# Kernel tuning notes

Measured on AMD Instinct MI355X. Metric: run time of the kernel, lower is better.

Reference implementation:

```python
import jax, jax.numpy as jnp
import numpy as np

B, T, D = 2, 512, 512
UNITS, H = 512, 8
DEPTH = UNITS // H  # 64


def setup_inputs() -> dict:
    key = jax.random.key(0)
    ks = jax.random.split(key, 16)
    s = 0.05  # keras 'random_normal' initializer stddev
    inp = {
        "query": jax.random.normal(ks[0], (B, T, D), jnp.float32),
        "key": jax.random.normal(ks[1], (B, T, D), jnp.float32),
        "value": jax.random.normal(ks[2], (B, T, D), jnp.float32),
        # input projections (Dense(units) with bias)
        "Wq": jax.random.normal(ks[3], (D, UNITS), jnp.float32) * s,
        "bq": jnp.zeros((UNITS,), jnp.float32),
        "Wk": jax.random.normal(ks[4], (D, UNITS), jnp.float32) * s,
        "bk": jnp.zeros((UNITS,), jnp.float32),
        "Wv": jax.random.normal(ks[5], (D, UNITS), jnp.float32) * s,
        "bv": jnp.zeros((UNITS,), jnp.float32),
        # per-head additive-attention params, stacked over heads
        "Wq_h": jax.random.normal(ks[6], (H, DEPTH, DEPTH), jnp.float32) * s,
        "Wk_h": jax.random.normal(ks[7], (H, DEPTH, DEPTH), jnp.float32) * s,
        "va_h": jax.random.normal(ks[8], (H, DEPTH), jnp.float32) * s,
        "b_h": jnp.zeros((H, DEPTH), jnp.float32),
        # output projection
        "Wo": jax.random.normal(ks[9], (UNITS, UNITS), jnp.float32) * s,
        "bo": jnp.zeros((UNITS,), jnp.float32),
    }
    return inp


def _split_heads(x):
    b = x.shape[0]
    return x.reshape(b, -1, H, DEPTH).transpose(0, 2, 1, 3)  # [B,H,T,depth]


def reference(query, key, value, Wq, bq, Wk, bk, Wv, bv,
              Wq_h, Wk_h, va_h, b_h, Wo, bo):
    Q = _split_heads(query @ Wq + bq)  # [B,H,T,d]
    K = _split_heads(key @ Wk + bk)    # [B,H,S,d]
    V = _split_heads(value @ Wv + bv)  # computed but unused, as in original

    # per-head linear maps for additive scores
    q = jnp.einsum("bhtd,hde->bhte", Q, Wq_h)
    k = jnp.einsum("bhsd,hde->bhse", K, Wk_h)
    # Bahdanau additive score: tanh(q_t + k_s + b) . v_a, summed over depth
    feat = jnp.tanh(q[:, :, :, None, :] + k[:, :, None, :, :]
                    + b_h[None, :, None, None, :])  # [B,H,T,S,d]
    score = jnp.einsum("bhtse,he->bhts", feat, va_h)  # [B,H,T,S]
    attn = jax.nn.softmax(score, axis=-1)
    # original multiplies by KEY (not value)
    heads = jnp.einsum("bhts,bhsd->bhtd", attn, K)  # [B,H,T,d]
    merged = heads.transpose(0, 2, 1, 3).reshape(query.shape[0], -1, UNITS)
    return merged @ Wo + bo
```

## Files before the change

### kernel.cpp

```cpp
#include <hip/hip_runtime.h>
#include <hip/hip_bf16.h>

#define T_SEQ 512
#define NH 8
#define DEPTH 64
#define UNITS_ 512
#define SCALE2 2.8853900817779268f
#define LOG2E 1.4426950408889634f

typedef __attribute__((ext_vector_type(8))) short short8;
typedef __attribute__((ext_vector_type(4))) float floatx4;

__global__ __launch_bounds__(256) void qk_head_fused(
    const float* __restrict__ query, const float* __restrict__ key,
    const float* __restrict__ Wq, const float* __restrict__ bq,
    const float* __restrict__ Wk, const float* __restrict__ bk,
    const float* __restrict__ Wq_h, const float* __restrict__ Wk_h,
    const float* __restrict__ bh,
    float* __restrict__ eq, float* __restrict__ ekT,
    __hip_bfloat16* __restrict__ KhT)
{
    __shared__ float S1[64][36];
    __shared__ float S2[64][68];

    const int tid = threadIdx.x;
    const int which = blockIdx.z;
    const int h  = blockIdx.x;
    const int m0 = blockIdx.y * 32;
    const int n0 = h * 64;
    const int b  = m0 >> 9;
    const int t0 = m0 & 511;
    const int bh_i = b * NH + h;

    const float* In   = which ? key : query;
    const float* W    = which ? Wk  : Wq;
    const float* bias = which ? bk  : bq;
    const float* Wp   = (which ? Wk_h : Wq_h) + h * 4096;

    const int arow = tid >> 3;
    const int acol = (tid & 7) * 4;
    const int bkk = tid >> 3;
    const int bn = (tid & 7) * 8;

    const int ti = tid >> 4;
    const int tj = tid & 15;

    const int wrow = tid >> 2;
    const int wcol = (tid & 3) * 16;
    float4 wh0 = *(const float4*)&Wp[wrow * 64 + wcol + 0];
    float4 wh1 = *(const float4*)&Wp[wrow * 64 + wcol + 4];
    float4 wh2 = *(const float4*)&Wp[wrow * 64 + wcol + 8];
    float4 wh3 = *(const float4*)&Wp[wrow * 64 + wcol + 12];

    float4 acc0 = make_float4(0.f, 0.f, 0.f, 0.f);
    float4 acc1 = make_float4(0.f, 0.f, 0.f, 0.f);

    float4 av  = *(const float4*)&In[(m0 + arow) * 512 + acol];
    float4 bv0 = *(const float4*)&W[bkk * 512 + n0 + bn];
    float4 bv1 = *(const float4*)&W[bkk * 512 + n0 + bn + 4];

    for (int k0 = 0; k0 < 512; k0 += 32) {
        __syncthreads();
        S1[acol + 0][arow] = av.x;
        S1[acol + 1][arow] = av.y;
        S1[acol + 2][arow] = av.z;
        S1[acol + 3][arow] = av.w;
        *(float4*)&S2[bkk][bn] = bv0;
        *(float4*)&S2[bkk][bn + 4] = bv1;
        __syncthreads();
        if (k0 + 32 < 512) {
            av  = *(const float4*)&In[(m0 + arow) * 512 + k0 + 32 + acol];
            bv0 = *(const float4*)&W[(k0 + 32 + bkk) * 512 + n0 + bn];
            bv1 = *(const float4*)&W[(k0 + 32 + bkk) * 512 + n0 + bn + 4];
        }
        #pragma unroll
        for (int kk = 0; kk < 32; ++kk) {
            float2 a2 = *(const float2*)&S1[kk][2 * ti];
            float4 b4 = *(const float4*)&S2[kk][4 * tj];
            acc0.x = fmaf(a2.x, b4.x, acc0.x);
            acc0.y = fmaf(a2.x, b4.y, acc0.y);
            acc0.z = fmaf(a2.x, b4.z, acc0.z);
            acc0.w = fmaf(a2.x, b4.w, acc0.w);
            acc1.x = fmaf(a2.y, b4.x, acc1.x);
            acc1.y = fmaf(a2.y, b4.y, acc1.y);
            acc1.z = fmaf(a2.y, b4.z, acc1.z);
            acc1.w = fmaf(a2.y, b4.w, acc1.w);
        }
    }

    float4 bb = *(const float4*)&bias[n0 + 4 * tj];
    __syncthreads();
    *(float2*)&S1[4 * tj + 0][2 * ti] = make_float2(acc0.x + bb.x, acc1.x + bb.x);
    *(float2*)&S1[4 * tj + 1][2 * ti] = make_float2(acc0.y + bb.y, acc1.y + bb.y);
    *(float2*)&S1[4 * tj + 2][2 * ti] = make_float2(acc0.z + bb.z, acc1.z + bb.z);
    *(float2*)&S1[4 * tj + 3][2 * ti] = make_float2(acc0.w + bb.w, acc1.w + bb.w);
    *(float4*)&S2[wrow][wcol + 0]  = wh0;
    *(float4*)&S2[wrow][wcol + 4]  = wh1;
    *(float4*)&S2[wrow][wcol + 8]  = wh2;
    *(float4*)&S2[wrow][wcol + 12] = wh3;
    __syncthreads();

    float4 qa0 = make_float4(0.f, 0.f, 0.f, 0.f);
    float4 qa1 = make_float4(0.f, 0.f, 0.f, 0.f);
    #pragma unroll 16
    for (int d = 0; d < 64; ++d) {
        float2 a2 = *(const float2*)&S1[d][2 * ti];
        float4 b4 = *(const float4*)&S2[d][4 * tj];
        qa0.x = fmaf(a2.x, b4.x, qa0.x);
        qa0.y = fmaf(a2.x, b4.y, qa0.y);
        qa0.z = fmaf(a2.x, b4.z, qa0.z);
        qa0.w = fmaf(a2.x, b4.w, qa0.w);
        qa1.x = fmaf(a2.y, b4.x, qa1.x);
        qa1.y = fmaf(a2.y, b4.y, qa1.y);
        qa1.z = fmaf(a2.y, b4.z, qa1.z);
        qa1.w = fmaf(a2.y, b4.w, qa1.w);
    }

    if (which == 0) {
        float* outp = eq + ((size_t)bh_i * 512 + t0) * 64;
        float4 o0, o1;
        o0.x = __builtin_amdgcn_exp2f(SCALE2 * qa0.x);
        o0.y = __builtin_amdgcn_exp2f(SCALE2 * qa0.y);
        o0.z = __builtin_amdgcn_exp2f(SCALE2 * qa0.z);
        o0.w = __builtin_amdgcn_exp2f(SCALE2 * qa0.w);
        o1.x = __builtin_amdgcn_exp2f(SCALE2 * qa1.x);
        o1.y = __builtin_amdgcn_exp2f(SCALE2 * qa1.y);
        o1.z = __builtin_amdgcn_exp2f(SCALE2 * qa1.z);
        o1.w = __builtin_amdgcn_exp2f(SCALE2 * qa1.w);
        *(float4*)&outp[(2 * ti + 0) * 64 + 4 * tj] = o0;
        *(float4*)&outp[(2 * ti + 1) * 64 + 4 * tj] = o1;
        return;
    }

    float4 bhv = *(const float4*)&bh[h * 64 + 4 * tj];
    __syncthreads();
    *(float2*)&S2[4 * tj + 0][2 * ti] = make_float2(
        __builtin_amdgcn_exp2f(SCALE2 * (qa0.x + bhv.x)),
        __builtin_amdgcn_exp2f(SCALE2 * (qa1.x + bhv.x)));
    *(float2*)&S2[4 * tj + 1][2 * ti] = make_float2(
        __builtin_amdgcn_exp2f(SCALE2 * (qa0.y + bhv.y)),
        __builtin_amdgcn_exp2f(SCALE2 * (qa1.y + bhv.y)));
    *(float2*)&S2[4 * tj + 2][2 * ti] = make_float2(
        __builtin_amdgcn_exp2f(SCALE2 * (qa0.z + bhv.z)),
        __builtin_amdgcn_exp2f(SCALE2 * (qa1.z + bhv.z)));
    *(float2*)&S2[4 * tj + 3][2 * ti] = make_float2(
        __builtin_amdgcn_exp2f(SCALE2 * (qa0.w + bhv.w)),
        __builtin_amdgcn_exp2f(SCALE2 * (qa1.w + bhv.w)));
    __syncthreads();

    const int dd = tid >> 2;
    const int sc = (tid & 3) * 8;
    float* ekp = ekT + ((size_t)bh_i * 64 + dd) * 512 + t0 + sc;
    *(float4*)&ekp[0] = *(float4*)&S2[dd][sc];
    *(float4*)&ekp[4] = *(float4*)&S2[dd][sc + 4];

    __hip_bfloat16* kp = KhT + ((size_t)bh_i * 64 + dd) * 512 + t0 + sc;
    union { short8 v; short s[8]; } pk;
    #pragma unroll
    for (int i = 0; i < 8; ++i) {
        __hip_bfloat16 b0 = __hip_bfloat16(S1[dd][sc + i]);
        pk.s[i] = *(short*)&b0;
    }
    *(short8*)kp = pk.v;
}

__global__ __launch_bounds__(512, 4) void attn_v4(
    const float* __restrict__ eq, const float* __restrict__ ekT,
    const __hip_bfloat16* __restrict__ KhT, const float* __restrict__ va_h,
    float* __restrict__ merged)
{
    __shared__ __hip_bfloat16 pA[16][520];
    __shared__ float wsum[8][8];

    const int tid = threadIdx.x;
    const int w = tid >> 6;
    const int l = tid & 63;
    const int bid = blockIdx.x;
    const int swz = (bid & 7) * 128 + (bid >> 3);
    const int t0 = (swz & 63) * 8;
    const int bh_i = swz >> 6;
    const int h = bh_i & 7;
    const int b = bh_i >> 3;

    {
        short8 z = {0, 0, 0, 0, 0, 0, 0, 0};
        *(short8*)&pA[8 + (tid >> 6)][(tid & 63) * 8] = z;
    }

    const float* eq_p = eq + ((size_t)bh_i * 512 + t0) * 64;
    const float* ekT_p = ekT + (size_t)bh_i * 64 * 512 + tid;
    const float* va_p = va_h + h * 64;

    float acc[8];
    #pragma unroll
    for (int t = 0; t < 8; ++t) acc[t] = 0.f;

    #pragma unroll
    for (int e0 = 0; e0 < 64; e0 += 16) {
        float ekv[16];
        #pragma unroll
        for (int j = 0; j < 16; ++j) ekv[j] = ekT_p[(e0 + j) * 512];
        float nv[16];
        #pragma unroll
        for (int j = 0; j < 16; ++j) nv[j] = -2.0f * va_p[e0 + j];
        #pragma unroll
        for (int t = 0; t < 8; ++t) {
            float a = acc[t];
            #pragma unroll
            for (int q = 0; q < 4; ++q) {
                float4 e4 = *(const float4*)&eq_p[t * 64 + e0 + q * 4];
                a = fmaf(nv[q * 4 + 0], __builtin_amdgcn_rcpf(fmaf(e4.x, ekv[q * 4 + 0], 1.0f)), a);
                a = fmaf(nv[q * 4 + 1], __builtin_amdgcn_rcpf(fmaf(e4.y, ekv[q * 4 + 1], 1.0f)), a);
                a = fmaf(nv[q * 4 + 2], __builtin_amdgcn_rcpf(fmaf(e4.z, ekv[q * 4 + 2], 1.0f)), a);
                a = fmaf(nv[q * 4 + 3], __builtin_amdgcn_rcpf(fmaf(e4.w, ekv[q * 4 + 3], 1.0f)), a);
            }
            acc[t] = a;
        }
    }

    float ev[8];
    #pragma unroll
    for (int t = 0; t < 8; ++t) {
        float s = __builtin_amdgcn_exp2f(acc[t] * LOG2E);
        ev[t] = s;
        #pragma unroll
        for (int off = 32; off > 0; off >>= 1) s += __shfl_xor(s, off, 64);
        if (l == 0) wsum[t][w] = s;
    }
    __syncthreads();
    #pragma unroll
    for (int t = 0; t < 8; ++t) {
        float4 s0 = *(float4*)&wsum[t][0];
        float4 s1 = *(float4*)&wsum[t][4];
        float inv = 1.0f / (((s0.x + s0.y) + (s0.z + s0.w)) + ((s1.x + s1.y) + (s1.z + s1.w)));
        pA[t][tid] = __hip_bfloat16(ev[t] * inv);
    }
    __syncthreads();

    if (w < 4) {
        const __hip_bfloat16* kp = KhT + (size_t)bh_i * 64 * 512
                                   + ((size_t)(w * 16 + (l & 15))) * 512 + (l >> 4) * 8;
        const __hip_bfloat16* ap = &pA[l & 15][(l >> 4) * 8];
        floatx4 oacc = {0.f, 0.f, 0.f, 0.f};
        #pragma unroll
        for (int kt = 0; kt < 16; ++kt) {
            short8 af = *(const short8*)(ap + kt * 32);
            short8 bf = *(const short8*)(kp + kt * 32);
            oacc = __builtin_amdgcn_mfma_f32_16x16x32_bf16(af, bf, oacc, 0, 0, 0);
        }
        if ((l >> 4) < 2) {
            const int row = (l >> 4) * 4;
            const int col = w * 16 + (l & 15);
            float* mp = merged + ((size_t)(b * 512 + t0 + row)) * 512 + h * 64 + col;
            #pragma unroll
            for (int r = 0; r < 4; ++r) mp[r * 512] = oacc[r];
        }
    }
}

__global__ __launch_bounds__(256) void gemm_out(
    const float* __restrict__ A, const float* __restrict__ W,
    const float* __restrict__ bias, float* __restrict__ C)
{
    __shared__ float As[32][36];
    __shared__ float Bs[32][36];

    const int tid = threadIdx.x;
    const int n0 = blockIdx.x * 32;
    const int m0 = blockIdx.y * 32;

    const int arow = tid >> 3;
    const int acol = (tid & 7) * 4;
    const int bkk = tid >> 3;
    const int bn = (tid & 7) * 4;

    const int ti = tid >> 4;
    const int tj = tid & 15;

    float2 acc0 = make_float2(0.f, 0.f);
    float2 acc1 = make_float2(0.f, 0.f);

    float4 av = *(const float4*)&A[(m0 + arow) * 512 + acol];
    float4 bv = *(const float4*)&W[bkk * 512 + n0 + bn];

    for (int k0 = 0; k0 < 512; k0 += 32) {
        __syncthreads();
        As[acol + 0][arow] = av.x;
        As[acol + 1][arow] = av.y;
        As[acol + 2][arow] = av.z;
        As[acol + 3][arow] = av.w;
        *(float4*)&Bs[bkk][bn] = bv;
        __syncthreads();
        if (k0 + 32 < 512) {
            av = *(const float4*)&A[(m0 + arow) * 512 + k0 + 32 + acol];
            bv = *(const float4*)&W[(k0 + 32 + bkk) * 512 + n0 + bn];
        }
        #pragma unroll
        for (int kk = 0; kk < 32; ++kk) {
            float2 a2 = *(const float2*)&As[kk][2 * ti];
            float2 b2 = *(const float2*)&Bs[kk][2 * tj];
            acc0.x = fmaf(a2.x, b2.x, acc0.x);
            acc0.y = fmaf(a2.x, b2.y, acc0.y);
            acc1.x = fmaf(a2.y, b2.x, acc1.x);
            acc1.y = fmaf(a2.y, b2.y, acc1.y);
        }
    }
    float2 bb = *(const float2*)&bias[n0 + 2 * tj];
    float2 o0 = make_float2(acc0.x + bb.x, acc0.y + bb.y);
    float2 o1 = make_float2(acc1.x + bb.x, acc1.y + bb.y);
    *(float2*)&C[(m0 + 2 * ti + 0) * 512 + n0 + 2 * tj] = o0;
    *(float2*)&C[(m0 + 2 * ti + 1) * 512 + n0 + 2 * tj] = o1;
}

extern "C" void kernel_launch(void* const* d_in, const int* in_sizes, int n_in,
                              void* d_out, int out_size, void* d_ws, size_t ws_size,
                              hipStream_t stream) {
    (void)in_sizes; (void)n_in; (void)out_size; (void)ws_size;
    const float* query = (const float*)d_in[0];
    const float* key   = (const float*)d_in[1];
    const float* Wq   = (const float*)d_in[3];
    const float* bq   = (const float*)d_in[4];
    const float* Wk   = (const float*)d_in[5];
    const float* bk   = (const float*)d_in[6];
    const float* Wq_h = (const float*)d_in[9];
    const float* Wk_h = (const float*)d_in[10];
    const float* va_h = (const float*)d_in[11];
    const float* b_h  = (const float*)d_in[12];
    const float* Wo   = (const float*)d_in[13];
    const float* bo   = (const float*)d_in[14];

    float* out = (float*)d_out;
    float* ws = (float*)d_ws;
    const int SZ = 1024 * 512;
    float* eqb     = ws;
    float* ekTb    = eqb + SZ;
    float* mergedb = ekTb + SZ;
    __hip_bfloat16* KhTb = (__hip_bfloat16*)(mergedb + SZ);

    qk_head_fused<<<dim3(8, 32, 2), 256, 0, stream>>>(query, key, Wq, bq, Wk, bk,
                                                      Wq_h, Wk_h, b_h,
                                                      eqb, ekTb, KhTb);
    attn_v4<<<dim3(1024, 1, 1), 512, 0, stream>>>(eqb, ekTb, KhTb, va_h, mergedb);
    gemm_out<<<dim3(16, 32, 1), 256, 0, stream>>>(mergedb, Wo, bo, out);
}
```

Before: 188.3 us.

## Use split-bf16 MFMA for projections and 16-row attention tiles

The input and output projection GEMMs move from scalar FP32 FMAs to bf16 MFMA. Each FP32 operand is split into hi and lo bf16 parts and three MFMA products are accumulated to keep close to FP32 accuracy. The attention kernel now handles 16 query rows per block instead of 8 and keeps all 64 key features in registers, so the key loads are reused across more rows. This comes at the cost of register pressure and extra conversion work, and the split-bf16 scheme adds a small numerical error.

```diff
diff --git a/kernel.cpp b/kernel.cpp
--- a/kernel.cpp
+++ b/kernel.cpp
@@ -8,10 +8,44 @@
 #define SCALE2 2.8853900817779268f
 #define LOG2E 1.4426950408889634f
 
+typedef __attribute__((ext_vector_type(4))) short bshort4;
 typedef __attribute__((ext_vector_type(8))) short short8;
 typedef __attribute__((ext_vector_type(4))) float floatx4;
 
-__global__ __launch_bounds__(256) void qk_head_fused(
+static __device__ __forceinline__ short bfh(float x) {
+    __hip_bfloat16 b(x);
+    return *(short*)&b;
+}
+static __device__ __forceinline__ float bff(short s) {
+    unsigned u = ((unsigned)(unsigned short)s) << 16;
+    float f;
+    __builtin_memcpy(&f, &u, 4);
+    return f;
+}
+static __device__ __forceinline__ void split4(float4 x, bshort4& h, bshort4& l) {
+    union { bshort4 v; short s[4]; } H, L;
+    float xs[4] = {x.x, x.y, x.z, x.w};
+    #pragma unroll
+    for (int i = 0; i < 4; ++i) {
+        short hh = bfh(xs[i]);
+        H.s[i] = hh;
+        L.s[i] = bfh(xs[i] - bff(hh));
+    }
+    h = H.v; l = L.v;
+}
+static __device__ __forceinline__ void split8(float4 x, float4 y, short8& h, short8& l) {
+    union { short8 v; short s[8]; } H, L;
+    float xs[8] = {x.x, x.y, x.z, x.w, y.x, y.y, y.z, y.w};
+    #pragma unroll
+    for (int i = 0; i < 8; ++i) {
+        short hh = bfh(xs[i]);
+        H.s[i] = hh;
+        L.s[i] = bfh(xs[i] - bff(hh));
+    }
+    h = H.v; l = L.v;
+}
+
+__global__ __launch_bounds__(512) void qk_head_mfma(
     const float* __restrict__ query, const float* __restrict__ key,
     const float* __restrict__ Wq, const float* __restrict__ bq,
     const float* __restrict__ Wk, const float* __restrict__ bk,
@@ -20,13 +54,18 @@
     float* __restrict__ eq, float* __restrict__ ekT,
     __hip_bfloat16* __restrict__ KhT)
 {
-    __shared__ float S1[64][36];
-    __shared__ float S2[64][68];
+    __shared__ __align__(16) short BUF[256 * 72];
+    short (*Ah)[72] = (short(*)[72])BUF;
+    short (*Al)[72] = (short(*)[72])(BUF + 64 * 72);
+    short (*Wh)[72] = (short(*)[72])(BUF + 128 * 72);
+    short (*Wl)[72] = (short(*)[72])(BUF + 192 * 72);
+    float (*S1)[68] = (float(*)[68])BUF;
+    float (*S2)[68] = (float(*)[68])(BUF + 8704);
 
     const int tid = threadIdx.x;
     const int which = blockIdx.z;
     const int h  = blockIdx.x;
-    const int m0 = blockIdx.y * 32;
+    const int m0 = blockIdx.y * 64;
     const int n0 = h * 64;
     const int b  = m0 >> 9;
     const int t0 = m0 & 511;
@@ -37,72 +76,93 @@
     const float* bias = which ? bk  : bq;
     const float* Wp   = (which ? Wk_h : Wq_h) + h * 4096;
 
+    const int wv = tid >> 6;
+    const int l  = tid & 63;
+    const int ms = (wv & 3) * 16;
+    const int ns = (wv >> 2) * 32;
+    const int fr = l & 15;
+    const int fq = l >> 4;
+
     const int arow = tid >> 3;
-    const int acol = (tid & 7) * 4;
-    const int bkk = tid >> 3;
-    const int bn = (tid & 7) * 8;
+    const int acol = (tid & 7) * 8;
+    const int wn   = tid & 63;
+    const int wkb  = (tid >> 6) * 8;
+
+    const int hwrow = tid >> 3;
+    const int hwcol = (tid & 7) * 8;
+    float4 whA = *(const float4*)&Wp[hwrow * 64 + hwcol];
+    float4 whB = *(const float4*)&Wp[hwrow * 64 + hwcol + 4];
+
+    const float bb0 = bias[n0 + ns + fr];
+    const float bb1 = bias[n0 + ns + 16 + fr];
+
+    floatx4 acc0 = {0.f, 0.f, 0.f, 0.f};
+    floatx4 acc1 = {0.f, 0.f, 0.f, 0.f};
+
+    float4 a0 = *(const float4*)&In[(m0 + arow) * 512 + acol];
+    float4 a1 = *(const float4*)&In[(m0 + arow) * 512 + acol + 4];
+    float wr[8];
+    #pragma unroll
+    for (int i = 0; i < 8; ++i) wr[i] = W[(wkb + i) * 512 + n0 + wn];
+
+    for (int k0 = 0; k0 < 512; k0 += 64) {
+        __syncthreads();
+        {
+            short8 h8, l8;
+            split8(a0, a1, h8, l8);
+            *(short8*)&Ah[arow][acol] = h8;
+            *(short8*)&Al[arow][acol] = l8;
+            union { short8 v; short s[8]; } WH, WL;
+            #pragma unroll
+            for (int i = 0; i < 8; ++i) {
+                short hh = bfh(wr[i]);
+                WH.s[i] = hh;
+                WL.s[i] = bfh(wr[i] - bff(hh));
+            }
+            *(short8*)&Wh[wn][wkb] = WH.v;
+            *(short8*)&Wl[wn][wkb] = WL.v;
+        }
+        __syncthreads();
+        if (k0 + 64 < 512) {
+            a0 = *(const float4*)&In[(m0 + arow) * 512 + k0 + 64 + acol];
+            a1 = *(const float4*)&In[(m0 + arow) * 512 + k0 + 64 + acol + 4];
+            #pragma unroll
+            for (int i = 0; i < 8; ++i)
+                wr[i] = W[(k0 + 64 + wkb + i) * 512 + n0 + wn];
+        }
+        #pragma unroll
+        for (int kc = 0; kc < 2; ++kc) {
+            const int ko = kc * 32 + fq * 8;
+            short8 ah  = *(const short8*)&Ah[ms + fr][ko];
+            short8 al  = *(const short8*)&Al[ms + fr][ko];
+            short8 w0h = *(const short8*)&Wh[ns + fr][ko];
+            short8 w0l = *(const short8*)&Wl[ns + fr][ko];
+            short8 w1h = *(const short8*)&Wh[ns + 16 + fr][ko];
+            short8 w1l = *(const short8*)&Wl[ns + 16 + fr][ko];
+            acc0 = __builtin_amdgcn_mfma_f32_16x16x32_bf16(ah, w0h, acc0, 0, 0, 0);
+            acc1 = __builtin_amdgcn_mfma_f32_16x16x32_bf16(ah, w1h, acc1, 0, 0, 0);
+            acc0 = __builtin_amdgcn_mfma_f32_16x16x32_bf16(ah, w0l, acc0, 0, 0, 0);
+            acc1 = __builtin_amdgcn_mfma_f32_16x16x32_bf16(ah, w1l, acc1, 0, 0, 0);
+            acc0 = __builtin_amdgcn_mfma_f32_16x16x32_bf16(al, w0h, acc0, 0, 0, 0);
+            acc1 = __builtin_amdgcn_mfma_f32_16x16x32_bf16(al, w1h, acc1, 0, 0, 0);
+        }
+    }
+
+    __syncthreads();
+    #pragma unroll
+    for (int r = 0; r < 4; ++r) {
+        S1[ns + fr][ms + fq * 4 + r]      = acc0[r] + bb0;
+        S1[ns + 16 + fr][ms + fq * 4 + r] = acc1[r] + bb1;
+    }
+    *(float4*)&S2[hwrow][hwcol]     = whA;
+    *(float4*)&S2[hwrow][hwcol + 4] = whB;
+    __syncthreads();
 
     const int ti = tid >> 4;
     const int tj = tid & 15;
-
-    const int wrow = tid >> 2;
-    const int wcol = (tid & 3) * 16;
-    float4 wh0 = *(const float4*)&Wp[wrow * 64 + wcol + 0];
-    float4 wh1 = *(const float4*)&Wp[wrow * 64 + wcol + 4];
-    float4 wh2 = *(const float4*)&Wp[wrow * 64 + wcol + 8];
-    float4 wh3 = *(const float4*)&Wp[wrow * 64 + wcol + 12];
-
-    float4 acc0 = make_float4(0.f, 0.f, 0.f, 0.f);
-    float4 acc1 = make_float4(0.f, 0.f, 0.f, 0.f);
-
-    float4 av  = *(const float4*)&In[(m0 + arow) * 512 + acol];
-    float4 bv0 = *(const float4*)&W[bkk * 512 + n0 + bn];
-    float4 bv1 = *(const float4*)&W[bkk * 512 + n0 + bn + 4];
-
-    for (int k0 = 0; k0 < 512; k0 += 32) {
-        __syncthreads();
-        S1[acol + 0][arow] = av.x;
-        S1[acol + 1][arow] = av.y;
-        S1[acol + 2][arow] = av.z;
-        S1[acol + 3][arow] = av.w;
-        *(float4*)&S2[bkk][bn] = bv0;
-        *(float4*)&S2[bkk][bn + 4] = bv1;
-        __syncthreads();
-        if (k0 + 32 < 512) {
-            av  = *(const float4*)&In[(m0 + arow) * 512 + k0 + 32 + acol];
-            bv0 = *(const float4*)&W[(k0 + 32 + bkk) * 512 + n0 + bn];
-            bv1 = *(const float4*)&W[(k0 + 32 + bkk) * 512 + n0 + bn + 4];
-        }
-        #pragma unroll
-        for (int kk = 0; kk < 32; ++kk) {
-            float2 a2 = *(const float2*)&S1[kk][2 * ti];
-            float4 b4 = *(const float4*)&S2[kk][4 * tj];
-            acc0.x = fmaf(a2.x, b4.x, acc0.x);
-            acc0.y = fmaf(a2.x, b4.y, acc0.y);
-            acc0.z = fmaf(a2.x, b4.z, acc0.z);
-            acc0.w = fmaf(a2.x, b4.w, acc0.w);
-            acc1.x = fmaf(a2.y, b4.x, acc1.x);
-            acc1.y = fmaf(a2.y, b4.y, acc1.y);
-            acc1.z = fmaf(a2.y, b4.z, acc1.z);
-            acc1.w = fmaf(a2.y, b4.w, acc1.w);
-        }
-    }
-
-    float4 bb = *(const float4*)&bias[n0 + 4 * tj];
-    __syncthreads();
-    *(float2*)&S1[4 * tj + 0][2 * ti] = make_float2(acc0.x + bb.x, acc1.x + bb.x);
-    *(float2*)&S1[4 * tj + 1][2 * ti] = make_float2(acc0.y + bb.y, acc1.y + bb.y);
-    *(float2*)&S1[4 * tj + 2][2 * ti] = make_float2(acc0.z + bb.z, acc1.z + bb.z);
-    *(float2*)&S1[4 * tj + 3][2 * ti] = make_float2(acc0.w + bb.w, acc1.w + bb.w);
-    *(float4*)&S2[wrow][wcol + 0]  = wh0;
-    *(float4*)&S2[wrow][wcol + 4]  = wh1;
-    *(float4*)&S2[wrow][wcol + 8]  = wh2;
-    *(float4*)&S2[wrow][wcol + 12] = wh3;
-    __syncthreads();
-
     float4 qa0 = make_float4(0.f, 0.f, 0.f, 0.f);
     float4 qa1 = make_float4(0.f, 0.f, 0.f, 0.f);
-    #pragma unroll 16
+    #pragma unroll 8
     for (int d = 0; d < 64; ++d) {
         float2 a2 = *(const float2*)&S1[d][2 * ti];
         float4 b4 = *(const float4*)&S2[d][4 * tj];
@@ -134,22 +194,18 @@
 
     float4 bhv = *(const float4*)&bh[h * 64 + 4 * tj];
     __syncthreads();
-    *(float2*)&S2[4 * tj + 0][2 * ti] = make_float2(
-        __builtin_amdgcn_exp2f(SCALE2 * (qa0.x + bhv.x)),
-        __builtin_amdgcn_exp2f(SCALE2 * (qa1.x + bhv.x)));
-    *(float2*)&S2[4 * tj + 1][2 * ti] = make_float2(
-        __builtin_amdgcn_exp2f(SCALE2 * (qa0.y + bhv.y)),
-        __builtin_amdgcn_exp2f(SCALE2 * (qa1.y + bhv.y)));
-    *(float2*)&S2[4 * tj + 2][2 * ti] = make_float2(
-        __builtin_amdgcn_exp2f(SCALE2 * (qa0.z + bhv.z)),
-        __builtin_amdgcn_exp2f(SCALE2 * (qa1.z + bhv.z)));
-    *(float2*)&S2[4 * tj + 3][2 * ti] = make_float2(
-        __builtin_amdgcn_exp2f(SCALE2 * (qa0.w + bhv.w)),
-        __builtin_amdgcn_exp2f(SCALE2 * (qa1.w + bhv.w)));
-    __syncthreads();
-
-    const int dd = tid >> 2;
-    const int sc = (tid & 3) * 8;
+    S2[4 * tj + 0][2 * ti + 0] = __builtin_amdgcn_exp2f(SCALE2 * (qa0.x + bhv.x));
+    S2[4 * tj + 0][2 * ti + 1] = __builtin_amdgcn_exp2f(SCALE2 * (qa1.x + bhv.x));
+    S2[4 * tj + 1][2 * ti + 0] = __builtin_amdgcn_exp2f(SCALE2 * (qa0.y + bhv.y));
+    S2[4 * tj + 1][2 * ti + 1] = __builtin_amdgcn_exp2f(SCALE2 * (qa1.y + bhv.y));
+    S2[4 * tj + 2][2 * ti + 0] = __builtin_amdgcn_exp2f(SCALE2 * (qa0.z + bhv.z));
+    S2[4 * tj + 2][2 * ti + 1] = __builtin_amdgcn_exp2f(SCALE2 * (qa1.z + bhv.z));
+    S2[4 * tj + 3][2 * ti + 0] = __builtin_amdgcn_exp2f(SCALE2 * (qa0.w + bhv.w));
+    S2[4 * tj + 3][2 * ti + 1] = __builtin_amdgcn_exp2f(SCALE2 * (qa1.w + bhv.w));
+    __syncthreads();
+
+    const int dd = tid >> 3;
+    const int sc = (tid & 7) * 8;
     float* ekp = ekT + ((size_t)bh_i * 64 + dd) * 512 + t0 + sc;
     *(float4*)&ekp[0] = *(float4*)&S2[dd][sc];
     *(float4*)&ekp[4] = *(float4*)&S2[dd][sc + 4];
@@ -157,71 +213,62 @@
     __hip_bfloat16* kp = KhT + ((size_t)bh_i * 64 + dd) * 512 + t0 + sc;
     union { short8 v; short s[8]; } pk;
     #pragma unroll
-    for (int i = 0; i < 8; ++i) {
-        __hip_bfloat16 b0 = __hip_bfloat16(S1[dd][sc + i]);
-        pk.s[i] = *(short*)&b0;
-    }
+    for (int i = 0; i < 8; ++i) pk.s[i] = bfh(S1[dd][sc + i]);
     *(short8*)kp = pk.v;
 }
 
-__global__ __launch_bounds__(512, 4) void attn_v4(
+__global__ __launch_bounds__(512, 4) void attn_v6(
     const float* __restrict__ eq, const float* __restrict__ ekT,
     const __hip_bfloat16* __restrict__ KhT, const float* __restrict__ va_h,
     float* __restrict__ merged)
 {
     __shared__ __hip_bfloat16 pA[16][520];
-    __shared__ float wsum[8][8];
+    __shared__ float wsum[16][8];
 
     const int tid = threadIdx.x;
     const int w = tid >> 6;
     const int l = tid & 63;
     const int bid = blockIdx.x;
-    const int swz = (bid & 7) * 128 + (bid >> 3);
-    const int t0 = (swz & 63) * 8;
-    const int bh_i = swz >> 6;
+    const int swz = (bid & 7) * 64 + (bid >> 3);
+    const int t0 = (swz & 31) * 16;
+    const int bh_i = swz >> 5;
     const int h = bh_i & 7;
     const int b = bh_i >> 3;
-
-    {
-        short8 z = {0, 0, 0, 0, 0, 0, 0, 0};
-        *(short8*)&pA[8 + (tid >> 6)][(tid & 63) * 8] = z;
-    }
 
     const float* eq_p = eq + ((size_t)bh_i * 512 + t0) * 64;
     const float* ekT_p = ekT + (size_t)bh_i * 64 * 512 + tid;
     const float* va_p = va_h + h * 64;
 
-    float acc[8];
-    #pragma unroll
-    for (int t = 0; t < 8; ++t) acc[t] = 0.f;
-
-    #pragma unroll
-    for (int e0 = 0; e0 < 64; e0 += 16) {
-        float ekv[16];
-        #pragma unroll
-        for (int j = 0; j < 16; ++j) ekv[j] = ekT_p[(e0 + j) * 512];
-        float nv[16];
-        #pragma unroll
-        for (int j = 0; j < 16; ++j) nv[j] = -2.0f * va_p[e0 + j];
-        #pragma unroll
-        for (int t = 0; t < 8; ++t) {
-            float a = acc[t];
-            #pragma unroll
-            for (int q = 0; q < 4; ++q) {
-                float4 e4 = *(const float4*)&eq_p[t * 64 + e0 + q * 4];
-                a = fmaf(nv[q * 4 + 0], __builtin_amdgcn_rcpf(fmaf(e4.x, ekv[q * 4 + 0], 1.0f)), a);
-                a = fmaf(nv[q * 4 + 1], __builtin_amdgcn_rcpf(fmaf(e4.y, ekv[q * 4 + 1], 1.0f)), a);
-                a = fmaf(nv[q * 4 + 2], __builtin_amdgcn_rcpf(fmaf(e4.z, ekv[q * 4 + 2], 1.0f)), a);
-                a = fmaf(nv[q * 4 + 3], __builtin_amdgcn_rcpf(fmaf(e4.w, ekv[q * 4 + 3], 1.0f)), a);
-            }
-            acc[t] = a;
-        }
-    }
-
-    float ev[8];
-    #pragma unroll
-    for (int t = 0; t < 8; ++t) {
-        float s = __builtin_amdgcn_exp2f(acc[t] * LOG2E);
+    float ekv[64];
+    #pragma unroll
+    for (int j = 0; j < 64; ++j) ekv[j] = ekT_p[j * 512];
+
+    float acc[16];
+    #pragma unroll
+    for (int t = 0; t < 16; ++t) {
+        float a0 = 0.f, a1 = 0.f;
+        #pragma unroll
+        for (int q = 0; q < 8; ++q) {
+            float4 e4 = *(const float4*)&eq_p[t * 64 + q * 8];
+            float4 f4 = *(const float4*)&eq_p[t * 64 + q * 8 + 4];
+            float4 v4 = *(const float4*)&va_p[q * 8];
+            float4 u4 = *(const float4*)&va_p[q * 8 + 4];
+            a0 = fmaf(v4.x, __builtin_amdgcn_rcpf(fmaf(e4.x, ekv[q * 8 + 0], 1.0f)), a0);
+            a0 = fmaf(v4.y, __builtin_amdgcn_rcpf(fmaf(e4.y, ekv[q * 8 + 1], 1.0f)), a0);
+            a0 = fmaf(v4.z, __builtin_amdgcn_rcpf(fmaf(e4.z, ekv[q * 8 + 2], 1.0f)), a0);
+            a0 = fmaf(v4.w, __builtin_amdgcn_rcpf(fmaf(e4.w, ekv[q * 8 + 3], 1.0f)), a0);
+            a1 = fmaf(u4.x, __builtin_amdgcn_rcpf(fmaf(f4.x, ekv[q * 8 + 4], 1.0f)), a1);
+            a1 = fmaf(u4.y, __builtin_amdgcn_rcpf(fmaf(f4.y, ekv[q * 8 + 5], 1.0f)), a1);
+            a1 = fmaf(u4.z, __builtin_amdgcn_rcpf(fmaf(f4.z, ekv[q * 8 + 6], 1.0f)), a1);
+            a1 = fmaf(u4.w, __builtin_amdgcn_rcpf(fmaf(f4.w, ekv[q * 8 + 7], 1.0f)), a1);
+        }
+        acc[t] = a0 + a1;
+    }
+
+    float ev[16];
+    #pragma unroll
+    for (int t = 0; t < 16; ++t) {
+        float s = __builtin_amdgcn_exp2f(-SCALE2 * acc[t]);
         ev[t] = s;
         #pragma unroll
         for (int off = 32; off > 0; off >>= 1) s += __shfl_xor(s, off, 64);
@@ -229,7 +276,7 @@
     }
     __syncthreads();
     #pragma unroll
-    for (int t = 0; t < 8; ++t) {
+    for (int t = 0; t < 16; ++t) {
         float4 s0 = *(float4*)&wsum[t][0];
         float4 s1 = *(float4*)&wsum[t][4];
         float inv = 1.0f / (((s0.x + s0.y) + (s0.z + s0.w)) + ((s1.x + s1.y) + (s1.z + s1.w)));
@@ -248,68 +295,89 @@
             short8 bf = *(const short8*)(kp + kt * 32);
             oacc = __builtin_amdgcn_mfma_f32_16x16x32_bf16(af, bf, oacc, 0, 0, 0);
         }
-        if ((l >> 4) < 2) {
-            const int row = (l >> 4) * 4;
-            const int col = w * 16 + (l & 15);
-            float* mp = merged + ((size_t)(b * 512 + t0 + row)) * 512 + h * 64 + col;
-            #pragma unroll
-            for (int r = 0; r < 4; ++r) mp[r * 512] = oacc[r];
-        }
-    }
-}
-
-__global__ __launch_bounds__(256) void gemm_out(
+        const int row = (l >> 4) * 4;
+        const int col = w * 16 + (l & 15);
+        float* mp = merged + ((size_t)(b * 512 + t0 + row)) * 512 + h * 64 + col;
+        #pragma unroll
+        for (int r = 0; r < 4; ++r) mp[r * 512] = oacc[r];
+    }
+}
+
+__global__ __launch_bounds__(512) void gemm_out_mfma(
     const float* __restrict__ A, const float* __restrict__ W,
     const float* __restrict__ bias, float* __restrict__ C)
 {
-    __shared__ float As[32][36];
-    __shared__ float Bs[32][36];
+    __shared__ __align__(16) short BUF[192 * 72];
+    short (*Ah)[72] = (short(*)[72])BUF;
+    short (*Al)[72] = (short(*)[72])(BUF + 32 * 72);
+    short (*Wh)[72] = (short(*)[72])(BUF + 64 * 72);
+    short (*Wl)[72] = (short(*)[72])(BUF + 128 * 72);
 
     const int tid = threadIdx.x;
-    const int n0 = blockIdx.x * 32;
+    const int n0 = blockIdx.x * 64;
     const int m0 = blockIdx.y * 32;
-
-    const int arow = tid >> 3;
-    const int acol = (tid & 7) * 4;
-    const int bkk = tid >> 3;
-    const int bn = (tid & 7) * 4;
-
-    const int ti = tid >> 4;
-    const int tj = tid & 15;
-
-    float2 acc0 = make_float2(0.f, 0.f);
-    float2 acc1 = make_float2(0.f, 0.f);
-
-    float4 av = *(const float4*)&A[(m0 + arow) * 512 + acol];
-    float4 bv = *(const float4*)&W[bkk * 512 + n0 + bn];
-
-    for (int k0 = 0; k0 < 512; k0 += 32) {
+    const int wv = tid >> 6;
+    const int l  = tid & 63;
+    const int ms = (wv & 1) * 16;
+    const int ns = (wv >> 1) * 16;
+    const int fr = l & 15;
+    const int fq = l >> 4;
+
+    const int arow = tid >> 4;
+    const int acol = (tid & 15) * 4;
+    const int wn   = tid & 63;
+    const int wkb  = (tid >> 6) * 8;
+
+    const float bb = bias[n0 + ns + fr];
+    floatx4 acc = {0.f, 0.f, 0.f, 0.f};
+
+    float4 a0 = *(const float4*)&A[(m0 + arow) * 512 + acol];
+    float wr[8];
+    #pragma unroll
+    for (int i = 0; i < 8; ++i) wr[i] = W[(wkb + i) * 512 + n0 + wn];
+
+    for (int k0 = 0; k0 < 512; k0 += 64) {
         __syncthreads();
-        As[acol + 0][arow] = av.x;
-        As[acol + 1][arow] = av.y;
-        As[acol + 2][arow] = av.z;
-        As[acol + 3][arow] = av.w;
-        *(float4*)&Bs[bkk][bn] = bv;
+        {
+            bshort4 h4, l4;
+            split4(a0, h4, l4);
+            *(bshort4*)&Ah[arow][acol] = h4;
+            *(bshort4*)&Al[arow][acol] = l4;
+            union { short8 v; short s[8]; } WH, WL;
+            #pragma unroll
+            for (int i = 0; i < 8; ++i) {
+                short hh = bfh(wr[i]);
+                WH.s[i] = hh;
+                WL.s[i] = bfh(wr[i] - bff(hh));
+            }
+            *(short8*)&Wh[wn][wkb] = WH.v;
+            *(short8*)&Wl[wn][wkb] = WL.v;
+        }
         __syncthreads();
-        if (k0 + 32 < 512) {
-            av = *(const float4*)&A[(m0 + arow) * 512 + k0 + 32 + acol];
-            bv = *(const float4*)&W[(k0 + 32 + bkk) * 512 + n0 + bn];
-        }
-        #pragma unroll
-        for (int kk = 0; kk < 32; ++kk) {
-            float2 a2 = *(const float2*)&As[kk][2 * ti];
-            float2 b2 = *(const float2*)&Bs[kk][2 * tj];
-            acc0.x = fmaf(a2.x, b2.x, acc0.x);
-            acc0.y = fmaf(a2.x, b2.y, acc0.y);
-            acc1.x = fmaf(a2.y, b2.x, acc1.x);
-            acc1.y = fmaf(a2.y, b2.y, acc1.y);
-        }
-    }
-    float2 bb = *(const float2*)&bias[n0 + 2 * tj];
-    float2 o0 = make_float2(acc0.x + bb.x, acc0.y + bb.y);
-    float2 o1 = make_float2(acc1.x + bb.x, acc1.y + bb.y);
-    *(float2*)&C[(m0 + 2 * ti + 0) * 512 + n0 + 2 * tj] = o0;
-    *(float2*)&C[(m0 + 2 * ti + 1) * 512 + n0 + 2 * tj] = o1;
+        if (k0 + 64 < 512) {
+            a0 = *(const float4*)&A[(m0 + arow) * 512 + k0 + 64 + acol];
+            #pragma unroll
+            for (int i = 0; i < 8; ++i)
+                wr[i] = W[(k0 + 64 + wkb + i) * 512 + n0 + wn];
+        }
+        #pragma unroll
+        for (int kc = 0; kc < 2; ++kc) {
+            const int ko = kc * 32 + fq * 8;
+            short8 ah = *(const short8*)&Ah[ms + fr][ko];
+            short8 al = *(const short8*)&Al[ms + fr][ko];
+            short8 wh = *(const short8*)&Wh[ns + fr][ko];
+            short8 wl = *(const short8*)&Wl[ns + fr][ko];
+            acc = __builtin_amdgcn_mfma_f32_16x16x32_bf16(ah, wh, acc, 0, 0, 0);
+            acc = __builtin_amdgcn_mfma_f32_16x16x32_bf16(ah, wl, acc, 0, 0, 0);
+            acc = __builtin_amdgcn_mfma_f32_16x16x32_bf16(al, wh, acc, 0, 0, 0);
+        }
+    }
+
+    const int mrow = m0 + ms + fq * 4;
+    const int ncol = n0 + ns + fr;
+    #pragma unroll
+    for (int r = 0; r < 4; ++r)
+        C[(size_t)(mrow + r) * 512 + ncol] = acc[r] + bb;
 }
 
 extern "C" void kernel_launch(void* const* d_in, const int* in_sizes, int n_in,
@@ -337,9 +405,9 @@
     float* mergedb = ekTb + SZ;
     __hip_bfloat16* KhTb = (__hip_bfloat16*)(mergedb + SZ);
 
-    qk_head_fused<<<dim3(8, 32, 2), 256, 0, stream>>>(query, key, Wq, bq, Wk, bk,
-                                                      Wq_h, Wk_h, b_h,
-                                                      eqb, ekTb, KhTb);
-    attn_v4<<<dim3(1024, 1, 1), 512, 0, stream>>>(eqb, ekTb, KhTb, va_h, mergedb);
-    gemm_out<<<dim3(16, 32, 1), 256, 0, stream>>>(mergedb, Wo, bo, out);
-}
+    qk_head_mfma<<<dim3(8, 16, 2), 512, 0, stream>>>(query, key, Wq, bq, Wk, bk,
+                                                     Wq_h, Wk_h, b_h,
+                                                     eqb, ekTb, KhTb);
+    attn_v6<<<dim3(512, 1, 1), 512, 0, stream>>>(eqb, ekTb, KhTb, va_h, mergedb);
+    gemm_out_mfma<<<dim3(8, 32, 1), 512, 0, stream>>>(mergedb, Wo, bo, out);
+}
```

Result: faster. 159.4 us (-15.3%).
